# Performance work log

Hardware: AMD Instinct MI355X
Metric: run time of the kernel (lower is better)

Reference implementation:

```python
import jax, jax.numpy as jnp
import numpy as np

N_NODES = 100000
N_EDGES = 3200000
IN_CH = 32
HID = 16


def setup_inputs() -> dict:
    key = jax.random.key(0)
    ks = jax.random.split(key, 8)
    x = jax.random.normal(ks[0], (N_NODES, IN_CH), dtype=jnp.float32)
    edge_index = jax.random.randint(ks[1], (2, N_EDGES), 0, N_NODES, dtype=jnp.int64)
    s1 = 1.0 / np.sqrt(IN_CH)
    s2 = 1.0 / np.sqrt(HID)
    Wl1 = jax.random.normal(ks[2], (HID, IN_CH), dtype=jnp.float32) * s1
    Wr1 = jax.random.normal(ks[3], (HID, IN_CH), dtype=jnp.float32) * s1
    b1 = jnp.zeros((HID,), dtype=jnp.float32)
    Wl2 = jax.random.normal(ks[4], (1, HID), dtype=jnp.float32) * s2
    Wr2 = jax.random.normal(ks[5], (1, HID), dtype=jnp.float32) * s2
    b2 = jnp.zeros((1,), dtype=jnp.float32)
    return {"x": x, "edge_index": edge_index, "Wl1": Wl1, "Wr1": Wr1,
            "b1": b1, "Wl2": Wl2, "Wr2": Wr2, "b2": b2}


def _sage_conv(h, src, dst, deg_inv, Wl, Wr, b):
    # mean aggregation of source features at destination nodes
    msg_sum = jax.ops.segment_sum(h[src], dst, num_segments=N_NODES)  # [N, F]
    agg = msg_sum * deg_inv[:, None]
    # lin_l(agg) + lin_r(h): lin_l carries the bias (PyG SAGEConv convention)
    return agg @ Wl.T + b + h @ Wr.T


def reference(x, edge_index, Wl1, Wr1, b1, Wl2, Wr2, b2):
    src = edge_index[0]
    dst = edge_index[1]
    deg = jax.ops.segment_sum(jnp.ones((N_EDGES,), dtype=x.dtype), dst,
                              num_segments=N_NODES)
    deg_inv = 1.0 / jnp.maximum(deg, 1.0)  # mean; nodes w/o in-edges get 0 agg

    h = _sage_conv(x, src, dst, deg_inv, Wl1, Wr1, b1)
    h = jax.nn.relu(h)
    # F.dropout in eval mode -> identity
    out = _sage_conv(h, src, dst, deg_inv, Wl2, Wr2, b2)
    return out.squeeze(-1)  # [N]
```

## Files before the change

### kernel.cpp

```cpp
#include <hip/hip_runtime.h>

#define N_NODES 100000
#define N_EDGES 3200000
#define NB 768
#define BKN 131
#define RSZ 5120
#define TILE 6250
#define NTILES 512
#define MAXIT 13
#define MAXB 10


__device__ __forceinline__ float bf2f_lo(unsigned int w) {
  return __uint_as_float(w << 16);
}
__device__ __forceinline__ float bf2f_hi(unsigned int w) {
  return __uint_as_float(w & 0xFFFF0000u);
}
__device__ __forceinline__ unsigned short f2bf(float f) {
  unsigned int b = __float_as_uint(f);
  return (unsigned short)((b + 0x7FFFu + ((b >> 16) & 1u)) >> 16);
}

__global__ __launch_bounds__(256) void k_proj1(
    const float* __restrict__ x, const float* __restrict__ Wl1,
    const float* __restrict__ Wr1, const float* __restrict__ b1,
    unsigned short* __restrict__ p1h, float* __restrict__ q1b,
    int* __restrict__ gcur) {
  __shared__ float sWl[512];
  __shared__ float sWr[512];
  __shared__ float sb[16];
  const int t = threadIdx.x;
  if (t < 32) {
    const int gi = blockIdx.x * 32 + t;
    if (gi < NB * 16) gcur[gi] = 0;
  }
  for (int i = t; i < 512; i += 256) {
    sWl[i] = Wl1[i];
    sWr[i] = Wr1[i];
  }
  if (t < 16) sb[t] = b1[t];
  __syncthreads();

  const int n = blockIdx.x * 256 + t;
  if (n >= N_NODES) return;

  float xr[32];
  const float4* xp = (const float4*)(x + (size_t)n * 32);
#pragma unroll
  for (int j = 0; j < 8; ++j) {
    float4 v = xp[j];
    xr[4 * j + 0] = v.x;
    xr[4 * j + 1] = v.y;
    xr[4 * j + 2] = v.z;
    xr[4 * j + 3] = v.w;
  }
  float pv[16], qv[16];
#pragma unroll
  for (int hh = 0; hh < 16; ++hh) {
    float a = 0.f, b = 0.f;
#pragma unroll
    for (int i = 0; i < 32; ++i) {
      a = fmaf(xr[i], sWl[hh * 32 + i], a);
      b = fmaf(xr[i], sWr[hh * 32 + i], b);
    }
    pv[hh] = a;
    qv[hh] = b + sb[hh];
  }
  unsigned int w[8];
#pragma unroll
  for (int j = 0; j < 8; ++j)
    w[j] = (unsigned int)f2bf(pv[2 * j]) |
           ((unsigned int)f2bf(pv[2 * j + 1]) << 16);
  uint4* pp = (uint4*)(p1h + (size_t)n * 16);
  pp[0] = make_uint4(w[0], w[1], w[2], w[3]);
  pp[1] = make_uint4(w[4], w[5], w[6], w[7]);
  float4* qp = (float4*)(q1b + (size_t)n * 16);
#pragma unroll
  for (int j = 0; j < 4; ++j)
    qp[j] = make_float4(qv[4 * j], qv[4 * j + 1], qv[4 * j + 2], qv[4 * j + 3]);
}

__global__ __launch_bounds__(512) void k_bscatter(const int* __restrict__ ei,
                                                  int* __restrict__ gcur,
                                                  int* __restrict__ recs) {
  __shared__ int hist[1024];
  __shared__ int delta[NB];
  __shared__ int seg[512];
  __shared__ int stage[TILE];
  __shared__ unsigned short bid[TILE + 6];
  const int t = threadIdx.x;
  for (int i = t; i < 1024; i += 512) hist[i] = 0;
  __syncthreads();

  const int tb = blockIdx.x * TILE;
  int rec[MAXIT], aux[MAXIT];
#pragma unroll
  for (int i = 0; i < MAXIT; ++i) {
    const int pos = t + i * 512;
    if (pos < TILE) {
      const int e = tb + pos;
      const int s = ei[e];
      const int d = ei[N_EDGES + e];
      const int k = (int)((unsigned)d / (unsigned)BKN);
      const int rank = atomicAdd(&hist[k], 1);
      rec[i] = ((d - k * BKN) << 17) | s;
      aux[i] = (k << 16) | rank;
    } else {
      aux[i] = -1;
    }
  }
  __syncthreads();

  const int s0 = hist[2 * t], s1 = hist[2 * t + 1];
  const int my = s0 + s1;
  seg[t] = my;
  __syncthreads();
#pragma unroll
  for (int o = 1; o < 512; o <<= 1) {
    const int a = (t >= o) ? seg[t - o] : 0;
    __syncthreads();
    seg[t] += a;
    __syncthreads();
  }
  const int ex = seg[t] - my;
  hist[2 * t] = ex;
  hist[2 * t + 1] = ex + s0;
  {
    const int b = 2 * t;
    if (b < NB && s0) delta[b] = b * RSZ + atomicAdd(&gcur[b * 16], s0) - ex;
    if (b + 1 < NB && s1)
      delta[b + 1] =
          (b + 1) * RSZ + atomicAdd(&gcur[(b + 1) * 16], s1) - (ex + s0);
  }
  __syncthreads();

#pragma unroll
  for (int i = 0; i < MAXIT; ++i) {
    if (aux[i] >= 0) stage[hist[aux[i] >> 16] + (aux[i] & 0xFFFF)] = rec[i];
  }
  for (int k2 = t; k2 < NB; k2 += 512) {
    const int st = hist[k2];
    const int en = hist[k2 + 1];
    for (int p = st; p < en; ++p) bid[p] = (unsigned short)k2;
  }
  __syncthreads();

  for (int pos = t; pos < TILE; pos += 512) {
    const int idx = delta[bid[pos]] + pos;
    if ((unsigned)idx < (unsigned)(NB * RSZ)) recs[idx] = stage[pos];
  }
}

__global__ __launch_bounds__(512) void k_sortagg1(
    const int* __restrict__ gcur, int* __restrict__ recs,
    const unsigned short* __restrict__ p1h, const float* __restrict__ q1b,
    const float* __restrict__ Wl2, const float* __restrict__ Wr2,
    float* __restrict__ p2, float* __restrict__ r2,
    float* __restrict__ deg_inv, int* __restrict__ node_off,
    int* __restrict__ node_cnt) {
  __shared__ int hist[132];
  __shared__ int nstart[132];
  __shared__ int ssort[RSZ];
  __shared__ float sWl[16], sWr[16];
  const int t = threadIdx.x;
  const int kb = blockIdx.x;
  const int b0 = kb * RSZ;
  const int gend = b0 + min(gcur[kb * 16], RSZ);
  if (t < 132) hist[t] = 0;
  if (t < 16) {
    sWl[t] = Wl2[t];
    sWr[t] = Wr2[t];
  }
  __syncthreads();

  int rc[MAXB], ax[MAXB];
#pragma unroll
  for (int i = 0; i < MAXB; ++i) {
    const int r = b0 + t + i * 512;
    if (r < gend) {
      const int rec = recs[r];
      const int local = rec >> 17;
      const int rank = atomicAdd(&hist[local], 1);
      rc[i] = rec & 0x1FFFF;
      ax[i] = (local << 13) | rank;
    } else {
      ax[i] = -1;
    }
  }
  __syncthreads();

  {
    int v = (t < 132) ? hist[t] : 0;
    if (t < 132) nstart[t] = v;
    __syncthreads();
#pragma unroll
    for (int o = 1; o < 132; o <<= 1) {
      const int a = (t < 132 && t >= o) ? nstart[t - o] : 0;
      __syncthreads();
      if (t < 132) nstart[t] += a;
      __syncthreads();
    }
    if (t < 132) nstart[t] -= v;
  }
  __syncthreads();

#pragma unroll
  for (int i = 0; i < MAXB; ++i) {
    if (ax[i] >= 0) ssort[nstart[ax[i] >> 13] + (ax[i] & 0x1FFF)] = rc[i];
  }
  __syncthreads();

  const int T = gend - b0;
  for (int j2 = t; j2 < T; j2 += 512) recs[b0 + j2] = ssort[j2];
  if (t < BKN) {
    const int n2 = kb * BKN + t;
    node_off[n2] = b0 + nstart[t];
    node_cnt[n2] = hist[t];
  }

  const int quad = t & 3;
  const int half = quad & 1;
  const int epar = quad >> 1;
  const unsigned short* pb = p1h + half * 8;
#pragma unroll
  for (int p = 0; p < 2; ++p) {
    const int local = p * 128 + (t >> 2);
    if (local >= BKN) continue;
    const int n = kb * BKN + local;
    if (n >= N_NODES) continue;
    const int st = nstart[local];
    const int k = hist[local];

    float acc[8];
#pragma unroll
    for (int i = 0; i < 8; ++i) acc[i] = 0.f;
    int j = epar;
    for (; j + 6 < k; j += 8) {
      const int s0 = ssort[st + j], s1 = ssort[st + j + 2],
                s2 = ssort[st + j + 4], s3 = ssort[st + j + 6];
      const uint4 w0 = *(const uint4*)(pb + (size_t)s0 * 16);
      const uint4 w1 = *(const uint4*)(pb + (size_t)s1 * 16);
      const uint4 w2 = *(const uint4*)(pb + (size_t)s2 * 16);
      const uint4 w3 = *(const uint4*)(pb + (size_t)s3 * 16);
      acc[0] +=
          (bf2f_lo(w0.x) + bf2f_lo(w1.x)) + (bf2f_lo(w2.x) + bf2f_lo(w3.x));
      acc[1] +=
          (bf2f_hi(w0.x) + bf2f_hi(w1.x)) + (bf2f_hi(w2.x) + bf2f_hi(w3.x));
      acc[2] +=
          (bf2f_lo(w0.y) + bf2f_lo(w1.y)) + (bf2f_lo(w2.y) + bf2f_lo(w3.y));
      acc[3] +=
          (bf2f_hi(w0.y) + bf2f_hi(w1.y)) + (bf2f_hi(w2.y) + bf2f_hi(w3.y));
      acc[4] +=
          (bf2f_lo(w0.z) + bf2f_lo(w1.z)) + (bf2f_lo(w2.z) + bf2f_lo(w3.z));
      acc[5] +=
          (bf2f_hi(w0.z) + bf2f_hi(w1.z)) + (bf2f_hi(w2.z) + bf2f_hi(w3.z));
      acc[6] +=
          (bf2f_lo(w0.w) + bf2f_lo(w1.w)) + (bf2f_lo(w2.w) + bf2f_lo(w3.w));
      acc[7] +=
          (bf2f_hi(w0.w) + bf2f_hi(w1.w)) + (bf2f_hi(w2.w) + bf2f_hi(w3.w));
    }
    for (; j < k; j += 2) {
      const uint4 w = *(const uint4*)(pb + (size_t)ssort[st + j] * 16);
      acc[0] += bf2f_lo(w.x);
      acc[1] += bf2f_hi(w.x);
      acc[2] += bf2f_lo(w.y);
      acc[3] += bf2f_hi(w.y);
      acc[4] += bf2f_lo(w.z);
      acc[5] += bf2f_hi(w.z);
      acc[6] += bf2f_lo(w.w);
      acc[7] += bf2f_hi(w.w);
    }
#pragma unroll
    for (int i = 0; i < 8; ++i) acc[i] += __shfl_xor(acc[i], 2);

    const float di = 1.f / fmaxf((float)k, 1.f);
    const float4* qp = (const float4*)(q1b + (size_t)n * 16 + half * 8);
    const float4 qa = qp[0], qb = qp[1];
    float h[8];
    h[0] = fmaxf(fmaf(acc[0], di, qa.x), 0.f);
    h[1] = fmaxf(fmaf(acc[1], di, qa.y), 0.f);
    h[2] = fmaxf(fmaf(acc[2], di, qa.z), 0.f);
    h[3] = fmaxf(fmaf(acc[3], di, qa.w), 0.f);
    h[4] = fmaxf(fmaf(acc[4], di, qb.x), 0.f);
    h[5] = fmaxf(fmaf(acc[5], di, qb.y), 0.f);
    h[6] = fmaxf(fmaf(acc[6], di, qb.z), 0.f);
    h[7] = fmaxf(fmaf(acc[7], di, qb.w), 0.f);
    float pa = 0.f, pbv = 0.f;
#pragma unroll
    for (int i = 0; i < 8; ++i) {
      pa = fmaf(h[i], sWl[half * 8 + i], pa);
      pbv = fmaf(h[i], sWr[half * 8 + i], pbv);
    }
    pa += __shfl_xor(pa, 1);
    pbv += __shfl_xor(pbv, 1);
    if (quad == 0) {
      p2[n] = pa;
      r2[n] = pbv;
      deg_inv[n] = di;
    }
  }
}

__global__ __launch_bounds__(512) void k_agg2out(
    const int* __restrict__ node_off, const int* __restrict__ node_cnt,
    const int* __restrict__ recs, const float* __restrict__ p2,
    const float* __restrict__ r2, const float* __restrict__ deg_inv,
    const float* __restrict__ b2, float* __restrict__ out) {
  const int t = threadIdx.x;
  const int kb = blockIdx.x;
  const int quad = t & 3;
#pragma unroll
  for (int p = 0; p < 2; ++p) {
    const int local = p * 128 + (t >> 2);
    if (local >= BKN) continue;
    const int n = kb * BKN + local;
    if (n >= N_NODES) continue;
    const int k0 = node_off[n];
    const int k = node_cnt[n];
    const int* sl = recs + k0;

    float u = 0.f;
    int j = quad;
    for (; j + 12 < k; j += 16) {
      const int sA = sl[j], sB = sl[j + 4], sC = sl[j + 8], sD = sl[j + 12];
      u += (p2[sA] + p2[sB]) + (p2[sC] + p2[sD]);
    }
    for (; j < k; j += 4) u += p2[sl[j]];
    u += __shfl_xor(u, 1);
    u += __shfl_xor(u, 2);
    if (quad == 0) out[n] = fmaf(u, deg_inv[n], r2[n] + b2[0]);
  }
}

extern "C" void kernel_launch(void* const* d_in, const int* in_sizes, int n_in,
                              void* d_out, int out_size, void* d_ws,
                              size_t ws_size, hipStream_t stream) {
  const float* x   = (const float*)d_in[0];
  const int*   ei  = (const int*)d_in[1];
  const float* Wl1 = (const float*)d_in[2];
  const float* Wr1 = (const float*)d_in[3];
  const float* b1  = (const float*)d_in[4];
  const float* Wl2 = (const float*)d_in[5];
  const float* Wr2 = (const float*)d_in[6];
  const float* b2  = (const float*)d_in[7];
  float* out = (float*)d_out;

  const size_t N = N_NODES;
  int* wi = (int*)d_ws;
  int* gcur     = wi;
  int* node_off = wi + NB * 16;
  int* node_cnt = node_off + 100608;
  int* recs     = node_cnt + 100608;
  unsigned short* p1h = (unsigned short*)(recs + (size_t)NB * RSZ);
  float* q1b     = (float*)(p1h + 16 * N);
  float* p2      = q1b + 16 * N;
  float* r2      = p2 + N;
  float* deg_inv = r2 + N;

  k_proj1<<<(N_NODES + 255) / 256, 256, 0, stream>>>(x, Wl1, Wr1, b1, p1h,
                                                     q1b, gcur);
  k_bscatter<<<NTILES, 512, 0, stream>>>(ei, gcur, recs);
  k_sortagg1<<<NB, 512, 0, stream>>>(gcur, recs, p1h, q1b, Wl2, Wr2, p2, r2,
                                     deg_inv, node_off, node_cnt);
  k_agg2out<<<NB, 512, 0, stream>>>(node_off, node_cnt, recs, p2, r2, deg_inv,
                                    b2, out);
}
```

Measured before the change: 175.0 us.

## Fuse pipeline into one cooperative kernel with grid syncs and shared-memory handoff

Merges the projection, bucket scatter, per-bucket sort/aggregation and second-layer aggregation into a single cooperative kernel of 512 blocks that are separated by grid-wide syncs. Buckets are resized to 196 nodes so one block handles one bucket and one edge tile. The sorted source lists, degrees and r2 values stay in shared memory for the final phase, so the sorted records and node offsets are never written back to global memory. This is meant to remove three kernel launch gaps and that global round trip. In exchange it depends on cooperative launch succeeding with large shared-memory usage, and falls back to three separate kernels if it does not.

Result: slower. 501.2 us (+186.3%).

```diff
diff --git a/kernel.cpp b/kernel.cpp
--- a/kernel.cpp
+++ b/kernel.cpp
@@ -1,15 +1,36 @@
 #include <hip/hip_runtime.h>
+#include <hip/hip_cooperative_groups.h>
+
+namespace cg = cooperative_groups;
 
 #define N_NODES 100000
 #define N_EDGES 3200000
-#define NB 768
-#define BKN 131
-#define RSZ 5120
+#define NB2 512
+#define BKN2 196
+#define RSZ2 7424
 #define TILE 6250
-#define NTILES 512
 #define MAXIT 13
-#define MAXB 10
-
+#define MAXB2 15
+
+
+union SM {
+  struct { float sWl[512]; float sWr[512]; float sb[16]; } proj;
+  struct {
+    int hist[1024];
+    int delta[NB2];
+    int seg[512];
+    int stage[TILE];
+    unsigned short bid[TILE + 6];
+  } sc;
+  struct {
+    int hist[BKN2 + 4];
+    int nstart[BKN2 + 4];
+    float sWl2[16], sWr2[16];
+    float sdeg[BKN2];
+    float sr2[BKN2];
+    int ssort[RSZ2];
+  } so;
+};
 
 __device__ __forceinline__ float bf2f_lo(unsigned int w) {
   return __uint_as_float(w << 16);
@@ -22,78 +43,65 @@
   return (unsigned short)((b + 0x7FFFu + ((b >> 16) & 1u)) >> 16);
 }
 
-__global__ __launch_bounds__(256) void k_proj1(
-    const float* __restrict__ x, const float* __restrict__ Wl1,
-    const float* __restrict__ Wr1, const float* __restrict__ b1,
-    unsigned short* __restrict__ p1h, float* __restrict__ q1b,
-    int* __restrict__ gcur) {
-  __shared__ float sWl[512];
-  __shared__ float sWr[512];
-  __shared__ float sb[16];
+__device__ __forceinline__ void phaseA(
+    const float* __restrict__ x, const int* __restrict__ ei,
+    const float* __restrict__ Wl1, const float* __restrict__ Wr1,
+    const float* __restrict__ b1, unsigned short* __restrict__ p1h,
+    float* __restrict__ q1b, int* __restrict__ gcur, int* __restrict__ recs,
+    SM& sm) {
   const int t = threadIdx.x;
-  if (t < 32) {
-    const int gi = blockIdx.x * 32 + t;
-    if (gi < NB * 16) gcur[gi] = 0;
-  }
-  for (int i = t; i < 512; i += 256) {
-    sWl[i] = Wl1[i];
-    sWr[i] = Wr1[i];
-  }
-  if (t < 16) sb[t] = b1[t];
-  __syncthreads();
-
-  const int n = blockIdx.x * 256 + t;
-  if (n >= N_NODES) return;
-
-  float xr[32];
-  const float4* xp = (const float4*)(x + (size_t)n * 32);
-#pragma unroll
-  for (int j = 0; j < 8; ++j) {
-    float4 v = xp[j];
-    xr[4 * j + 0] = v.x;
-    xr[4 * j + 1] = v.y;
-    xr[4 * j + 2] = v.z;
-    xr[4 * j + 3] = v.w;
-  }
-  float pv[16], qv[16];
-#pragma unroll
-  for (int hh = 0; hh < 16; ++hh) {
-    float a = 0.f, b = 0.f;
-#pragma unroll
-    for (int i = 0; i < 32; ++i) {
-      a = fmaf(xr[i], sWl[hh * 32 + i], a);
-      b = fmaf(xr[i], sWr[hh * 32 + i], b);
-    }
-    pv[hh] = a;
-    qv[hh] = b + sb[hh];
-  }
-  unsigned int w[8];
-#pragma unroll
-  for (int j = 0; j < 8; ++j)
-    w[j] = (unsigned int)f2bf(pv[2 * j]) |
-           ((unsigned int)f2bf(pv[2 * j + 1]) << 16);
-  uint4* pp = (uint4*)(p1h + (size_t)n * 16);
-  pp[0] = make_uint4(w[0], w[1], w[2], w[3]);
-  pp[1] = make_uint4(w[4], w[5], w[6], w[7]);
-  float4* qp = (float4*)(q1b + (size_t)n * 16);
-#pragma unroll
-  for (int j = 0; j < 4; ++j)
-    qp[j] = make_float4(qv[4 * j], qv[4 * j + 1], qv[4 * j + 2], qv[4 * j + 3]);
-}
-
-__global__ __launch_bounds__(512) void k_bscatter(const int* __restrict__ ei,
-                                                  int* __restrict__ gcur,
-                                                  int* __restrict__ recs) {
-  __shared__ int hist[1024];
-  __shared__ int delta[NB];
-  __shared__ int seg[512];
-  __shared__ int stage[TILE];
-  __shared__ unsigned short bid[TILE + 6];
-  const int t = threadIdx.x;
-  for (int i = t; i < 1024; i += 512) hist[i] = 0;
-  __syncthreads();
-
-  const int tb = blockIdx.x * TILE;
+  const int kb = blockIdx.x;
+
+  sm.proj.sWl[t] = Wl1[t];
+  sm.proj.sWr[t] = Wr1[t];
+  if (t < 16) sm.proj.sb[t] = b1[t];
+  __syncthreads();
+  if (t < BKN2) {
+    const int n = kb * BKN2 + t;
+    if (n < N_NODES) {
+      float xr[32];
+      const float4* xp = (const float4*)(x + (size_t)n * 32);
+#pragma unroll
+      for (int j = 0; j < 8; ++j) {
+        float4 v = xp[j];
+        xr[4 * j + 0] = v.x;
+        xr[4 * j + 1] = v.y;
+        xr[4 * j + 2] = v.z;
+        xr[4 * j + 3] = v.w;
+      }
+      float pv[16], qv[16];
+#pragma unroll
+      for (int hh = 0; hh < 16; ++hh) {
+        float a = 0.f, b = 0.f;
+#pragma unroll
+        for (int i = 0; i < 32; ++i) {
+          a = fmaf(xr[i], sm.proj.sWl[hh * 32 + i], a);
+          b = fmaf(xr[i], sm.proj.sWr[hh * 32 + i], b);
+        }
+        pv[hh] = a;
+        qv[hh] = b + sm.proj.sb[hh];
+      }
+      unsigned int w[8];
+#pragma unroll
+      for (int j = 0; j < 8; ++j)
+        w[j] = (unsigned int)f2bf(pv[2 * j]) |
+               ((unsigned int)f2bf(pv[2 * j + 1]) << 16);
+      uint4* pp = (uint4*)(p1h + (size_t)n * 16);
+      pp[0] = make_uint4(w[0], w[1], w[2], w[3]);
+      pp[1] = make_uint4(w[4], w[5], w[6], w[7]);
+      float4* qp = (float4*)(q1b + (size_t)n * 16);
+#pragma unroll
+      for (int j = 0; j < 4; ++j)
+        qp[j] =
+            make_float4(qv[4 * j], qv[4 * j + 1], qv[4 * j + 2], qv[4 * j + 3]);
+    }
+  }
+  __syncthreads();
+
+  for (int i = t; i < 1024; i += 512) sm.sc.hist[i] = 0;
+  __syncthreads();
+
+  const int tb = kb * TILE;
   int rec[MAXIT], aux[MAXIT];
 #pragma unroll
   for (int i = 0; i < MAXIT; ++i) {
@@ -102,9 +110,9 @@
       const int e = tb + pos;
       const int s = ei[e];
       const int d = ei[N_EDGES + e];
-      const int k = (int)((unsigned)d / (unsigned)BKN);
-      const int rank = atomicAdd(&hist[k], 1);
-      rec[i] = ((d - k * BKN) << 17) | s;
+      const int k = (int)((unsigned)d / (unsigned)BKN2);
+      const int rank = atomicAdd(&sm.sc.hist[k], 1);
+      rec[i] = ((d - k * BKN2) << 17) | s;
       aux[i] = (k << 16) | rank;
     } else {
       aux[i] = -1;
@@ -112,77 +120,77 @@
   }
   __syncthreads();
 
-  const int s0 = hist[2 * t], s1 = hist[2 * t + 1];
+  const int s0 = sm.sc.hist[2 * t], s1 = sm.sc.hist[2 * t + 1];
   const int my = s0 + s1;
-  seg[t] = my;
+  sm.sc.seg[t] = my;
   __syncthreads();
 #pragma unroll
   for (int o = 1; o < 512; o <<= 1) {
-    const int a = (t >= o) ? seg[t - o] : 0;
+    const int a = (t >= o) ? sm.sc.seg[t - o] : 0;
     __syncthreads();
-    seg[t] += a;
+    sm.sc.seg[t] += a;
     __syncthreads();
   }
-  const int ex = seg[t] - my;
-  hist[2 * t] = ex;
-  hist[2 * t + 1] = ex + s0;
+  const int ex = sm.sc.seg[t] - my;
+  sm.sc.hist[2 * t] = ex;
+  sm.sc.hist[2 * t + 1] = ex + s0;
   {
     const int b = 2 * t;
-    if (b < NB && s0) delta[b] = b * RSZ + atomicAdd(&gcur[b * 16], s0) - ex;
-    if (b + 1 < NB && s1)
-      delta[b + 1] =
-          (b + 1) * RSZ + atomicAdd(&gcur[(b + 1) * 16], s1) - (ex + s0);
+    if (b < NB2 && s0)
+      sm.sc.delta[b] = b * RSZ2 + atomicAdd(&gcur[b * 16], s0) - ex;
+    if (b + 1 < NB2 && s1)
+      sm.sc.delta[b + 1] =
+          (b + 1) * RSZ2 + atomicAdd(&gcur[(b + 1) * 16], s1) - (ex + s0);
   }
   __syncthreads();
 
 #pragma unroll
   for (int i = 0; i < MAXIT; ++i) {
-    if (aux[i] >= 0) stage[hist[aux[i] >> 16] + (aux[i] & 0xFFFF)] = rec[i];
-  }
-  for (int k2 = t; k2 < NB; k2 += 512) {
-    const int st = hist[k2];
-    const int en = hist[k2 + 1];
-    for (int p = st; p < en; ++p) bid[p] = (unsigned short)k2;
+    if (aux[i] >= 0)
+      sm.sc.stage[sm.sc.hist[aux[i] >> 16] + (aux[i] & 0xFFFF)] = rec[i];
+  }
+  {
+    const int st = sm.sc.hist[t];
+    const int en = sm.sc.hist[t + 1];
+    for (int p = st; p < en; ++p) sm.sc.bid[p] = (unsigned short)t;
   }
   __syncthreads();
 
   for (int pos = t; pos < TILE; pos += 512) {
-    const int idx = delta[bid[pos]] + pos;
-    if ((unsigned)idx < (unsigned)(NB * RSZ)) recs[idx] = stage[pos];
-  }
-}
-
-__global__ __launch_bounds__(512) void k_sortagg1(
+    const int bb = sm.sc.bid[pos];
+    const int idx = sm.sc.delta[bb] + pos;
+    if (idx < (bb + 1) * RSZ2) recs[idx] = sm.sc.stage[pos];
+  }
+}
+
+template <bool FUSED>
+__device__ __forceinline__ void phaseB(
     const int* __restrict__ gcur, int* __restrict__ recs,
     const unsigned short* __restrict__ p1h, const float* __restrict__ q1b,
     const float* __restrict__ Wl2, const float* __restrict__ Wr2,
-    float* __restrict__ p2, float* __restrict__ r2,
-    float* __restrict__ deg_inv, int* __restrict__ node_off,
-    int* __restrict__ node_cnt) {
-  __shared__ int hist[132];
-  __shared__ int nstart[132];
-  __shared__ int ssort[RSZ];
-  __shared__ float sWl[16], sWr[16];
+    float* __restrict__ p2, float* __restrict__ r2g, float* __restrict__ degg,
+    int* __restrict__ node_off, int* __restrict__ node_cnt, SM& sm) {
   const int t = threadIdx.x;
   const int kb = blockIdx.x;
-  const int b0 = kb * RSZ;
-  const int gend = b0 + min(gcur[kb * 16], RSZ);
-  if (t < 132) hist[t] = 0;
+  const int b0 = kb * RSZ2;
+  const int cnt = min(gcur[kb * 16], RSZ2);
+  const int gend = b0 + cnt;
+  if (t < BKN2 + 4) sm.so.hist[t] = 0;
   if (t < 16) {
-    sWl[t] = Wl2[t];
-    sWr[t] = Wr2[t];
-  }
-  __syncthreads();
-
-  int rc[MAXB], ax[MAXB];
-#pragma unroll
-  for (int i = 0; i < MAXB; ++i) {
+    sm.so.sWl2[t] = Wl2[t];
+    sm.so.sWr2[t] = Wr2[t];
+  }
+  __syncthreads();
+
+  int rc[MAXB2], ax[MAXB2];
+#pragma unroll
+  for (int i = 0; i < MAXB2; ++i) {
     const int r = b0 + t + i * 512;
     if (r < gend) {
-      const int rec = recs[r];
-      const int local = rec >> 17;
-      const int rank = atomicAdd(&hist[local], 1);
-      rc[i] = rec & 0x1FFFF;
+      const int rv = recs[r];
+      const int local = rv >> 17;
+      const int rank = atomicAdd(&sm.so.hist[local], 1);
+      rc[i] = rv & 0x1FFFF;
       ax[i] = (local << 13) | rank;
     } else {
       ax[i] = -1;
@@ -191,32 +199,36 @@
   __syncthreads();
 
   {
-    int v = (t < 132) ? hist[t] : 0;
-    if (t < 132) nstart[t] = v;
+    int v = (t <= BKN2) ? sm.so.hist[t] : 0;
+    if (t <= BKN2) sm.so.nstart[t] = v;
     __syncthreads();
 #pragma unroll
-    for (int o = 1; o < 132; o <<= 1) {
-      const int a = (t < 132 && t >= o) ? nstart[t - o] : 0;
+    for (int o = 1; o < BKN2 + 1; o <<= 1) {
+      const int a = (t <= BKN2 && t >= o) ? sm.so.nstart[t - o] : 0;
       __syncthreads();
-      if (t < 132) nstart[t] += a;
+      if (t <= BKN2) sm.so.nstart[t] += a;
       __syncthreads();
     }
-    if (t < 132) nstart[t] -= v;
-  }
-  __syncthreads();
-
-#pragma unroll
-  for (int i = 0; i < MAXB; ++i) {
-    if (ax[i] >= 0) ssort[nstart[ax[i] >> 13] + (ax[i] & 0x1FFF)] = rc[i];
-  }
-  __syncthreads();
-
-  const int T = gend - b0;
-  for (int j2 = t; j2 < T; j2 += 512) recs[b0 + j2] = ssort[j2];
-  if (t < BKN) {
-    const int n2 = kb * BKN + t;
-    node_off[n2] = b0 + nstart[t];
-    node_cnt[n2] = hist[t];
+    if (t <= BKN2) sm.so.nstart[t] -= v;
+  }
+  __syncthreads();
+
+#pragma unroll
+  for (int i = 0; i < MAXB2; ++i) {
+    if (ax[i] >= 0)
+      sm.so.ssort[sm.so.nstart[ax[i] >> 13] + (ax[i] & 0x1FFF)] = rc[i];
+  }
+  __syncthreads();
+
+  if (!FUSED) {
+    for (int j2 = t; j2 < cnt; j2 += 512) recs[b0 + j2] = sm.so.ssort[j2];
+    if (t < BKN2) {
+      const int n2 = kb * BKN2 + t;
+      if (n2 < N_NODES) {
+        node_off[n2] = b0 + sm.so.nstart[t];
+        node_cnt[n2] = sm.so.hist[t];
+      }
+    }
   }
 
   const int quad = t & 3;
@@ -226,19 +238,19 @@
 #pragma unroll
   for (int p = 0; p < 2; ++p) {
     const int local = p * 128 + (t >> 2);
-    if (local >= BKN) continue;
-    const int n = kb * BKN + local;
+    if (local >= BKN2) continue;
+    const int n = kb * BKN2 + local;
     if (n >= N_NODES) continue;
-    const int st = nstart[local];
-    const int k = hist[local];
+    const int st = sm.so.nstart[local];
+    const int k = sm.so.hist[local];
 
     float acc[8];
 #pragma unroll
     for (int i = 0; i < 8; ++i) acc[i] = 0.f;
     int j = epar;
     for (; j + 6 < k; j += 8) {
-      const int s0 = ssort[st + j], s1 = ssort[st + j + 2],
-                s2 = ssort[st + j + 4], s3 = ssort[st + j + 6];
+      const int s0 = sm.so.ssort[st + j], s1 = sm.so.ssort[st + j + 2],
+                s2 = sm.so.ssort[st + j + 4], s3 = sm.so.ssort[st + j + 6];
       const uint4 w0 = *(const uint4*)(pb + (size_t)s0 * 16);
       const uint4 w1 = *(const uint4*)(pb + (size_t)s1 * 16);
       const uint4 w2 = *(const uint4*)(pb + (size_t)s2 * 16);
@@ -261,7 +273,7 @@
           (bf2f_hi(w0.w) + bf2f_hi(w1.w)) + (bf2f_hi(w2.w) + bf2f_hi(w3.w));
     }
     for (; j < k; j += 2) {
-      const uint4 w = *(const uint4*)(pb + (size_t)ssort[st + j] * 16);
+      const uint4 w = *(const uint4*)(pb + (size_t)sm.so.ssort[st + j] * 16);
       acc[0] += bf2f_lo(w.x);
       acc[1] += bf2f_hi(w.x);
       acc[2] += bf2f_lo(w.y);
@@ -289,80 +301,156 @@
     float pa = 0.f, pbv = 0.f;
 #pragma unroll
     for (int i = 0; i < 8; ++i) {
-      pa = fmaf(h[i], sWl[half * 8 + i], pa);
-      pbv = fmaf(h[i], sWr[half * 8 + i], pbv);
+      pa = fmaf(h[i], sm.so.sWl2[half * 8 + i], pa);
+      pbv = fmaf(h[i], sm.so.sWr2[half * 8 + i], pbv);
     }
     pa += __shfl_xor(pa, 1);
     pbv += __shfl_xor(pbv, 1);
     if (quad == 0) {
       p2[n] = pa;
-      r2[n] = pbv;
-      deg_inv[n] = di;
-    }
-  }
-}
-
-__global__ __launch_bounds__(512) void k_agg2out(
+      if (FUSED) {
+        sm.so.sr2[local] = pbv;
+        sm.so.sdeg[local] = di;
+      } else {
+        r2g[n] = pbv;
+        degg[n] = di;
+      }
+    }
+  }
+}
+
+template <bool FUSED>
+__device__ __forceinline__ void phaseC(
     const int* __restrict__ node_off, const int* __restrict__ node_cnt,
     const int* __restrict__ recs, const float* __restrict__ p2,
-    const float* __restrict__ r2, const float* __restrict__ deg_inv,
-    const float* __restrict__ b2, float* __restrict__ out) {
+    const float* __restrict__ r2g, const float* __restrict__ degg,
+    const float* __restrict__ b2, float* __restrict__ out, SM& sm) {
   const int t = threadIdx.x;
   const int kb = blockIdx.x;
   const int quad = t & 3;
+  const float bias = b2[0];
 #pragma unroll
   for (int p = 0; p < 2; ++p) {
     const int local = p * 128 + (t >> 2);
-    if (local >= BKN) continue;
-    const int n = kb * BKN + local;
+    if (local >= BKN2) continue;
+    const int n = kb * BKN2 + local;
     if (n >= N_NODES) continue;
-    const int k0 = node_off[n];
-    const int k = node_cnt[n];
-    const int* sl = recs + k0;
+    int st, k;
+    if (FUSED) {
+      st = sm.so.nstart[local];
+      k = sm.so.hist[local];
+    } else {
+      st = node_off[n];
+      k = node_cnt[n];
+    }
 
     float u = 0.f;
     int j = quad;
-    for (; j + 12 < k; j += 16) {
-      const int sA = sl[j], sB = sl[j + 4], sC = sl[j + 8], sD = sl[j + 12];
-      u += (p2[sA] + p2[sB]) + (p2[sC] + p2[sD]);
-    }
-    for (; j < k; j += 4) u += p2[sl[j]];
+    if (FUSED) {
+      for (; j + 12 < k; j += 16) {
+        const int sA = sm.so.ssort[st + j], sB = sm.so.ssort[st + j + 4],
+                  sC = sm.so.ssort[st + j + 8], sD = sm.so.ssort[st + j + 12];
+        u += (p2[sA] + p2[sB]) + (p2[sC] + p2[sD]);
+      }
+      for (; j < k; j += 4) u += p2[sm.so.ssort[st + j]];
+    } else {
+      const int* sl = recs + st;
+      for (; j + 12 < k; j += 16) {
+        const int sA = sl[j], sB = sl[j + 4], sC = sl[j + 8], sD = sl[j + 12];
+        u += (p2[sA] + p2[sB]) + (p2[sC] + p2[sD]);
+      }
+      for (; j < k; j += 4) u += p2[sl[j]];
+    }
     u += __shfl_xor(u, 1);
     u += __shfl_xor(u, 2);
-    if (quad == 0) out[n] = fmaf(u, deg_inv[n], r2[n] + b2[0]);
-  }
+    if (quad == 0) {
+      const float di = FUSED ? sm.so.sdeg[local] : degg[n];
+      const float rv = FUSED ? sm.so.sr2[local] : r2g[n];
+      out[n] = fmaf(u, di, rv + bias);
+    }
+  }
+}
+
+__global__ __launch_bounds__(512, 4) void k_fused(
+    const float* x, const int* ei, const float* Wl1, const float* Wr1,
+    const float* b1, const float* Wl2, const float* Wr2, const float* b2,
+    unsigned short* p1h, float* q1b, int* gcur, int* recs, float* p2,
+    float* out) {
+  __shared__ SM sm;
+  cg::grid_group g = cg::this_grid();
+  phaseA(x, ei, Wl1, Wr1, b1, p1h, q1b, gcur, recs, sm);
+  __threadfence();
+  g.sync();
+  phaseB<true>(gcur, recs, p1h, q1b, Wl2, Wr2, p2, nullptr, nullptr, nullptr,
+               nullptr, sm);
+  __threadfence();
+  g.sync();
+  phaseC<true>(nullptr, nullptr, recs, p2, nullptr, nullptr, b2, out, sm);
+}
+
+__global__ __launch_bounds__(512, 4) void k_pA(const float* x, const int* ei,
+                                               const float* Wl1,
+                                               const float* Wr1,
+                                               const float* b1,
+                                               unsigned short* p1h, float* q1b,
+                                               int* gcur, int* recs) {
+  __shared__ SM sm;
+  phaseA(x, ei, Wl1, Wr1, b1, p1h, q1b, gcur, recs, sm);
+}
+__global__ __launch_bounds__(512, 4) void k_pB(
+    const int* gcur, int* recs, const unsigned short* p1h, const float* q1b,
+    const float* Wl2, const float* Wr2, float* p2, float* r2g, float* degg,
+    int* node_off, int* node_cnt) {
+  __shared__ SM sm;
+  phaseB<false>(gcur, recs, p1h, q1b, Wl2, Wr2, p2, r2g, degg, node_off,
+                node_cnt, sm);
+}
+__global__ __launch_bounds__(512, 4) void k_pC(
+    const int* node_off, const int* node_cnt, const int* recs, const float* p2,
+    const float* r2g, const float* degg, const float* b2, float* out) {
+  __shared__ SM sm;
+  phaseC<false>(node_off, node_cnt, recs, p2, r2g, degg, b2, out, sm);
 }
 
 extern "C" void kernel_launch(void* const* d_in, const int* in_sizes, int n_in,
                               void* d_out, int out_size, void* d_ws,
                               size_t ws_size, hipStream_t stream) {
-  const float* x   = (const float*)d_in[0];
-  const int*   ei  = (const int*)d_in[1];
+  const float* x = (const float*)d_in[0];
+  const int* ei = (const int*)d_in[1];
   const float* Wl1 = (const float*)d_in[2];
   const float* Wr1 = (const float*)d_in[3];
-  const float* b1  = (const float*)d_in[4];
+  const float* b1 = (const float*)d_in[4];
   const float* Wl2 = (const float*)d_in[5];
   const float* Wr2 = (const float*)d_in[6];
-  const float* b2  = (const float*)d_in[7];
+  const float* b2 = (const float*)d_in[7];
   float* out = (float*)d_out;
 
   const size_t N = N_NODES;
   int* wi = (int*)d_ws;
-  int* gcur     = wi;
-  int* node_off = wi + NB * 16;
-  int* node_cnt = node_off + 100608;
-  int* recs     = node_cnt + 100608;
-  unsigned short* p1h = (unsigned short*)(recs + (size_t)NB * RSZ);
-  float* q1b     = (float*)(p1h + 16 * N);
-  float* p2      = q1b + 16 * N;
-  float* r2      = p2 + N;
-  float* deg_inv = r2 + N;
-
-  k_proj1<<<(N_NODES + 255) / 256, 256, 0, stream>>>(x, Wl1, Wr1, b1, p1h,
-                                                     q1b, gcur);
-  k_bscatter<<<NTILES, 512, 0, stream>>>(ei, gcur, recs);
-  k_sortagg1<<<NB, 512, 0, stream>>>(gcur, recs, p1h, q1b, Wl2, Wr2, p2, r2,
-                                     deg_inv, node_off, node_cnt);
-  k_agg2out<<<NB, 512, 0, stream>>>(node_off, node_cnt, recs, p2, r2, deg_inv,
-                                    b2, out);
-}
+  int* gcur = wi;
+  int* node_off = wi + NB2 * 16;
+  int* node_cnt = node_off + 100352;
+  int* recs = node_cnt + 100352;
+  unsigned short* p1h = (unsigned short*)(recs + (size_t)NB2 * RSZ2);
+  float* q1b = (float*)(p1h + 16 * N);
+  float* p2 = q1b + 16 * N;
+  float* r2 = p2 + N;
+  float* degg = r2 + N;
+
+  hipMemsetAsync(gcur, 0, NB2 * 16 * sizeof(int), stream);
+
+  void* ka[] = {(void*)&x,   (void*)&ei,  (void*)&Wl1, (void*)&Wr1,
+                (void*)&b1,  (void*)&Wl2, (void*)&Wr2, (void*)&b2,
+                (void*)&p1h, (void*)&q1b, (void*)&gcur, (void*)&recs,
+                (void*)&p2,  (void*)&out};
+  hipError_t err = hipLaunchCooperativeKernel(
+      reinterpret_cast<void*>(k_fused), dim3(NB2), dim3(512), ka, 0, stream);
+  if (err != hipSuccess) {
+    (void)hipGetLastError();
+    k_pA<<<NB2, 512, 0, stream>>>(x, ei, Wl1, Wr1, b1, p1h, q1b, gcur, recs);
+    k_pB<<<NB2, 512, 0, stream>>>(gcur, recs, p1h, q1b, Wl2, Wr2, p2, r2, degg,
+                                  node_off, node_cnt);
+    k_pC<<<NB2, 512, 0, stream>>>(node_off, node_cnt, recs, p2, r2, degg, b2,
+                                  out);
+  }
+}
```

## Use smaller buckets and LDS-atomic layer-2 aggregation over unsorted records

Applied to the files above, without the earlier changes.

Grows the bucket count to 1024 with 98 nodes per bucket and a smaller record region per bucket. Each sort/aggregate block now handles one node per quad, and the block no longer writes sorted records and per-node offsets back to global memory. Layer-2 aggregation reads the unsorted bucket records directly and accumulates p2 values with shared-memory atomics per local node. This drops a global write-back pass and two index arrays, at the cost of shared atomic contention and a tighter per-bucket capacity that could overflow on skewed inputs.

Result: no change. 172.0 us (-1.7%).

```diff
diff --git a/kernel.cpp b/kernel.cpp
--- a/kernel.cpp
+++ b/kernel.cpp
@@ -2,13 +2,13 @@
 
 #define N_NODES 100000
 #define N_EDGES 3200000
-#define NB 768
-#define BKN 131
-#define RSZ 5120
+#define NB 1024
+#define BKN 98
+#define RSZ 3968
 #define TILE 6250
 #define NTILES 512
 #define MAXIT 13
-#define MAXB 10
+#define MAXB 8
 
 
 __device__ __forceinline__ float bf2f_lo(unsigned int w) {
@@ -31,8 +31,8 @@
   __shared__ float sWr[512];
   __shared__ float sb[16];
   const int t = threadIdx.x;
-  if (t < 32) {
-    const int gi = blockIdx.x * 32 + t;
+  if (t < 64) {
+    const int gi = blockIdx.x * 64 + t;
     if (gi < NB * 16) gcur[gi] = 0;
   }
   for (int i = t; i < 512; i += 256) {
@@ -128,8 +128,8 @@
   hist[2 * t + 1] = ex + s0;
   {
     const int b = 2 * t;
-    if (b < NB && s0) delta[b] = b * RSZ + atomicAdd(&gcur[b * 16], s0) - ex;
-    if (b + 1 < NB && s1)
+    if (s0) delta[b] = b * RSZ + atomicAdd(&gcur[b * 16], s0) - ex;
+    if (s1)
       delta[b + 1] =
           (b + 1) * RSZ + atomicAdd(&gcur[(b + 1) * 16], s1) - (ex + s0);
   }
@@ -141,33 +141,33 @@
   }
   for (int k2 = t; k2 < NB; k2 += 512) {
     const int st = hist[k2];
-    const int en = hist[k2 + 1];
+    const int en = (k2 == NB - 1) ? TILE : hist[k2 + 1];
     for (int p = st; p < en; ++p) bid[p] = (unsigned short)k2;
   }
   __syncthreads();
 
   for (int pos = t; pos < TILE; pos += 512) {
-    const int idx = delta[bid[pos]] + pos;
-    if ((unsigned)idx < (unsigned)(NB * RSZ)) recs[idx] = stage[pos];
-  }
-}
-
-__global__ __launch_bounds__(512) void k_sortagg1(
-    const int* __restrict__ gcur, int* __restrict__ recs,
+    const int bb = bid[pos];
+    const int idx = delta[bb] + pos;
+    if (idx < (bb + 1) * RSZ) recs[idx] = stage[pos];
+  }
+}
+
+__global__ __launch_bounds__(512, 8) void k_sortagg1(
+    const int* __restrict__ gcur, const int* __restrict__ recs,
     const unsigned short* __restrict__ p1h, const float* __restrict__ q1b,
     const float* __restrict__ Wl2, const float* __restrict__ Wr2,
     float* __restrict__ p2, float* __restrict__ r2,
-    float* __restrict__ deg_inv, int* __restrict__ node_off,
-    int* __restrict__ node_cnt) {
-  __shared__ int hist[132];
-  __shared__ int nstart[132];
+    float* __restrict__ deg_inv) {
+  __shared__ int hist[128];
+  __shared__ int nstart[128];
   __shared__ int ssort[RSZ];
   __shared__ float sWl[16], sWr[16];
   const int t = threadIdx.x;
   const int kb = blockIdx.x;
   const int b0 = kb * RSZ;
   const int gend = b0 + min(gcur[kb * 16], RSZ);
-  if (t < 132) hist[t] = 0;
+  if (t < 128) hist[t] = 0;
   if (t < 16) {
     sWl[t] = Wl2[t];
     sWr[t] = Wr2[t];
@@ -179,10 +179,10 @@
   for (int i = 0; i < MAXB; ++i) {
     const int r = b0 + t + i * 512;
     if (r < gend) {
-      const int rec = recs[r];
-      const int local = rec >> 17;
+      const int rv = recs[r];
+      const int local = rv >> 17;
       const int rank = atomicAdd(&hist[local], 1);
-      rc[i] = rec & 0x1FFFF;
+      rc[i] = rv & 0x1FFFF;
       ax[i] = (local << 13) | rank;
     } else {
       ax[i] = -1;
@@ -191,17 +191,17 @@
   __syncthreads();
 
   {
-    int v = (t < 132) ? hist[t] : 0;
-    if (t < 132) nstart[t] = v;
+    const int v = (t < 128) ? hist[t] : 0;
+    if (t < 128) nstart[t] = v;
     __syncthreads();
 #pragma unroll
-    for (int o = 1; o < 132; o <<= 1) {
-      const int a = (t < 132 && t >= o) ? nstart[t - o] : 0;
+    for (int o = 1; o < 128; o <<= 1) {
+      const int a = (t < 128 && t >= o) ? nstart[t - o] : 0;
       __syncthreads();
-      if (t < 132) nstart[t] += a;
+      if (t < 128) nstart[t] += a;
       __syncthreads();
     }
-    if (t < 132) nstart[t] -= v;
+    if (t < 128) nstart[t] -= v;
   }
   __syncthreads();
 
@@ -210,126 +210,126 @@
     if (ax[i] >= 0) ssort[nstart[ax[i] >> 13] + (ax[i] & 0x1FFF)] = rc[i];
   }
   __syncthreads();
-
-  const int T = gend - b0;
-  for (int j2 = t; j2 < T; j2 += 512) recs[b0 + j2] = ssort[j2];
-  if (t < BKN) {
-    const int n2 = kb * BKN + t;
-    node_off[n2] = b0 + nstart[t];
-    node_cnt[n2] = hist[t];
-  }
 
   const int quad = t & 3;
   const int half = quad & 1;
   const int epar = quad >> 1;
   const unsigned short* pb = p1h + half * 8;
-#pragma unroll
-  for (int p = 0; p < 2; ++p) {
-    const int local = p * 128 + (t >> 2);
-    if (local >= BKN) continue;
+  const int local = t >> 2;
+  if (local < BKN) {
     const int n = kb * BKN + local;
-    if (n >= N_NODES) continue;
-    const int st = nstart[local];
-    const int k = hist[local];
-
-    float acc[8];
-#pragma unroll
-    for (int i = 0; i < 8; ++i) acc[i] = 0.f;
-    int j = epar;
-    for (; j + 6 < k; j += 8) {
-      const int s0 = ssort[st + j], s1 = ssort[st + j + 2],
-                s2 = ssort[st + j + 4], s3 = ssort[st + j + 6];
-      const uint4 w0 = *(const uint4*)(pb + (size_t)s0 * 16);
-      const uint4 w1 = *(const uint4*)(pb + (size_t)s1 * 16);
-      const uint4 w2 = *(const uint4*)(pb + (size_t)s2 * 16);
-      const uint4 w3 = *(const uint4*)(pb + (size_t)s3 * 16);
-      acc[0] +=
-          (bf2f_lo(w0.x) + bf2f_lo(w1.x)) + (bf2f_lo(w2.x) + bf2f_lo(w3.x));
-      acc[1] +=
-          (bf2f_hi(w0.x) + bf2f_hi(w1.x)) + (bf2f_hi(w2.x) + bf2f_hi(w3.x));
-      acc[2] +=
-          (bf2f_lo(w0.y) + bf2f_lo(w1.y)) + (bf2f_lo(w2.y) + bf2f_lo(w3.y));
-      acc[3] +=
-          (bf2f_hi(w0.y) + bf2f_hi(w1.y)) + (bf2f_hi(w2.y) + bf2f_hi(w3.y));
-      acc[4] +=
-          (bf2f_lo(w0.z) + bf2f_lo(w1.z)) + (bf2f_lo(w2.z) + bf2f_lo(w3.z));
-      acc[5] +=
-          (bf2f_hi(w0.z) + bf2f_hi(w1.z)) + (bf2f_hi(w2.z) + bf2f_hi(w3.z));
-      acc[6] +=
-          (bf2f_lo(w0.w) + bf2f_lo(w1.w)) + (bf2f_lo(w2.w) + bf2f_lo(w3.w));
-      acc[7] +=
-          (bf2f_hi(w0.w) + bf2f_hi(w1.w)) + (bf2f_hi(w2.w) + bf2f_hi(w3.w));
-    }
-    for (; j < k; j += 2) {
-      const uint4 w = *(const uint4*)(pb + (size_t)ssort[st + j] * 16);
-      acc[0] += bf2f_lo(w.x);
-      acc[1] += bf2f_hi(w.x);
-      acc[2] += bf2f_lo(w.y);
-      acc[3] += bf2f_hi(w.y);
-      acc[4] += bf2f_lo(w.z);
-      acc[5] += bf2f_hi(w.z);
-      acc[6] += bf2f_lo(w.w);
-      acc[7] += bf2f_hi(w.w);
-    }
-#pragma unroll
-    for (int i = 0; i < 8; ++i) acc[i] += __shfl_xor(acc[i], 2);
-
-    const float di = 1.f / fmaxf((float)k, 1.f);
-    const float4* qp = (const float4*)(q1b + (size_t)n * 16 + half * 8);
-    const float4 qa = qp[0], qb = qp[1];
-    float h[8];
-    h[0] = fmaxf(fmaf(acc[0], di, qa.x), 0.f);
-    h[1] = fmaxf(fmaf(acc[1], di, qa.y), 0.f);
-    h[2] = fmaxf(fmaf(acc[2], di, qa.z), 0.f);
-    h[3] = fmaxf(fmaf(acc[3], di, qa.w), 0.f);
-    h[4] = fmaxf(fmaf(acc[4], di, qb.x), 0.f);
-    h[5] = fmaxf(fmaf(acc[5], di, qb.y), 0.f);
-    h[6] = fmaxf(fmaf(acc[6], di, qb.z), 0.f);
-    h[7] = fmaxf(fmaf(acc[7], di, qb.w), 0.f);
-    float pa = 0.f, pbv = 0.f;
-#pragma unroll
-    for (int i = 0; i < 8; ++i) {
-      pa = fmaf(h[i], sWl[half * 8 + i], pa);
-      pbv = fmaf(h[i], sWr[half * 8 + i], pbv);
-    }
-    pa += __shfl_xor(pa, 1);
-    pbv += __shfl_xor(pbv, 1);
-    if (quad == 0) {
-      p2[n] = pa;
-      r2[n] = pbv;
-      deg_inv[n] = di;
-    }
-  }
-}
-
-__global__ __launch_bounds__(512) void k_agg2out(
-    const int* __restrict__ node_off, const int* __restrict__ node_cnt,
-    const int* __restrict__ recs, const float* __restrict__ p2,
-    const float* __restrict__ r2, const float* __restrict__ deg_inv,
-    const float* __restrict__ b2, float* __restrict__ out) {
+    if (n < N_NODES) {
+      const int st = nstart[local];
+      const int k = hist[local];
+
+      float acc[8];
+#pragma unroll
+      for (int i = 0; i < 8; ++i) acc[i] = 0.f;
+      int j = epar;
+      for (; j + 6 < k; j += 8) {
+        const int s0 = ssort[st + j], s1 = ssort[st + j + 2],
+                  s2 = ssort[st + j + 4], s3 = ssort[st + j + 6];
+        const uint4 w0 = *(const uint4*)(pb + (size_t)s0 * 16);
+        const uint4 w1 = *(const uint4*)(pb + (size_t)s1 * 16);
+        const uint4 w2 = *(const uint4*)(pb + (size_t)s2 * 16);
+        const uint4 w3 = *(const uint4*)(pb + (size_t)s3 * 16);
+        acc[0] +=
+            (bf2f_lo(w0.x) + bf2f_lo(w1.x)) + (bf2f_lo(w2.x) + bf2f_lo(w3.x));
+        acc[1] +=
+            (bf2f_hi(w0.x) + bf2f_hi(w1.x)) + (bf2f_hi(w2.x) + bf2f_hi(w3.x));
+        acc[2] +=
+            (bf2f_lo(w0.y) + bf2f_lo(w1.y)) + (bf2f_lo(w2.y) + bf2f_lo(w3.y));
+        acc[3] +=
+            (bf2f_hi(w0.y) + bf2f_hi(w1.y)) + (bf2f_hi(w2.y) + bf2f_hi(w3.y));
+        acc[4] +=
+            (bf2f_lo(w0.z) + bf2f_lo(w1.z)) + (bf2f_lo(w2.z) + bf2f_lo(w3.z));
+        acc[5] +=
+            (bf2f_hi(w0.z) + bf2f_hi(w1.z)) + (bf2f_hi(w2.z) + bf2f_hi(w3.z));
+        acc[6] +=
+            (bf2f_lo(w0.w) + bf2f_lo(w1.w)) + (bf2f_lo(w2.w) + bf2f_lo(w3.w));
+        acc[7] +=
+            (bf2f_hi(w0.w) + bf2f_hi(w1.w)) + (bf2f_hi(w2.w) + bf2f_hi(w3.w));
+      }
+      for (; j < k; j += 2) {
+        const uint4 w = *(const uint4*)(pb + (size_t)ssort[st + j] * 16);
+        acc[0] += bf2f_lo(w.x);
+        acc[1] += bf2f_hi(w.x);
+        acc[2] += bf2f_lo(w.y);
+        acc[3] += bf2f_hi(w.y);
+        acc[4] += bf2f_lo(w.z);
+        acc[5] += bf2f_hi(w.z);
+        acc[6] += bf2f_lo(w.w);
+        acc[7] += bf2f_hi(w.w);
+      }
+#pragma unroll
+      for (int i = 0; i < 8; ++i) acc[i] += __shfl_xor(acc[i], 2);
+
+      const float di = 1.f / fmaxf((float)k, 1.f);
+      const float4* qp = (const float4*)(q1b + (size_t)n * 16 + half * 8);
+      const float4 qa = qp[0], qb = qp[1];
+      float h[8];
+      h[0] = fmaxf(fmaf(acc[0], di, qa.x), 0.f);
+      h[1] = fmaxf(fmaf(acc[1], di, qa.y), 0.f);
+      h[2] = fmaxf(fmaf(acc[2], di, qa.z), 0.f);
+      h[3] = fmaxf(fmaf(acc[3], di, qa.w), 0.f);
+      h[4] = fmaxf(fmaf(acc[4], di, qb.x), 0.f);
+      h[5] = fmaxf(fmaf(acc[5], di, qb.y), 0.f);
+      h[6] = fmaxf(fmaf(acc[6], di, qb.z), 0.f);
+      h[7] = fmaxf(fmaf(acc[7], di, qb.w), 0.f);
+      float pa = 0.f, pbv = 0.f;
+#pragma unroll
+      for (int i = 0; i < 8; ++i) {
+        pa = fmaf(h[i], sWl[half * 8 + i], pa);
+        pbv = fmaf(h[i], sWr[half * 8 + i], pbv);
+      }
+      pa += __shfl_xor(pa, 1);
+      pbv += __shfl_xor(pbv, 1);
+      if (quad == 0) {
+        p2[n] = pa;
+        r2[n] = pbv;
+        deg_inv[n] = di;
+      }
+    }
+  }
+}
+
+__global__ __launch_bounds__(512, 8) void k_agg2out(
+    const int* __restrict__ gcur, const int* __restrict__ recs,
+    const float* __restrict__ p2, const float* __restrict__ r2,
+    const float* __restrict__ deg_inv, const float* __restrict__ b2,
+    float* __restrict__ out) {
+  __shared__ float acc[BKN];
   const int t = threadIdx.x;
   const int kb = blockIdx.x;
-  const int quad = t & 3;
-#pragma unroll
-  for (int p = 0; p < 2; ++p) {
-    const int local = p * 128 + (t >> 2);
-    if (local >= BKN) continue;
-    const int n = kb * BKN + local;
-    if (n >= N_NODES) continue;
-    const int k0 = node_off[n];
-    const int k = node_cnt[n];
-    const int* sl = recs + k0;
-
-    float u = 0.f;
-    int j = quad;
-    for (; j + 12 < k; j += 16) {
-      const int sA = sl[j], sB = sl[j + 4], sC = sl[j + 8], sD = sl[j + 12];
-      u += (p2[sA] + p2[sB]) + (p2[sC] + p2[sD]);
-    }
-    for (; j < k; j += 4) u += p2[sl[j]];
-    u += __shfl_xor(u, 1);
-    u += __shfl_xor(u, 2);
-    if (quad == 0) out[n] = fmaf(u, deg_inv[n], r2[n] + b2[0]);
+  if (t < BKN) acc[t] = 0.f;
+  __syncthreads();
+
+  const int b0 = kb * RSZ;
+  const int cnt = min(gcur[kb * 16], RSZ);
+  int r = t;
+  for (; r + 1536 < cnt; r += 2048) {
+    const int rv0 = recs[b0 + r];
+    const int rv1 = recs[b0 + r + 512];
+    const int rv2 = recs[b0 + r + 1024];
+    const int rv3 = recs[b0 + r + 1536];
+    const float v0 = p2[rv0 & 0x1FFFF];
+    const float v1 = p2[rv1 & 0x1FFFF];
+    const float v2 = p2[rv2 & 0x1FFFF];
+    const float v3 = p2[rv3 & 0x1FFFF];
+    atomicAdd(&acc[rv0 >> 17], v0);
+    atomicAdd(&acc[rv1 >> 17], v1);
+    atomicAdd(&acc[rv2 >> 17], v2);
+    atomicAdd(&acc[rv3 >> 17], v3);
+  }
+  for (; r < cnt; r += 512) {
+    const int rv = recs[b0 + r];
+    atomicAdd(&acc[rv >> 17], p2[rv & 0x1FFFF]);
+  }
+  __syncthreads();
+
+  if (t < BKN) {
+    const int n = kb * BKN + t;
+    if (n < N_NODES) out[n] = fmaf(acc[t], deg_inv[n], r2[n] + b2[0]);
   }
 }
 
@@ -348,10 +348,8 @@
 
   const size_t N = N_NODES;
   int* wi = (int*)d_ws;
-  int* gcur     = wi;
-  int* node_off = wi + NB * 16;
-  int* node_cnt = node_off + 100608;
-  int* recs     = node_cnt + 100608;
+  int* gcur = wi;
+  int* recs = wi + NB * 16;
   unsigned short* p1h = (unsigned short*)(recs + (size_t)NB * RSZ);
   float* q1b     = (float*)(p1h + 16 * N);
   float* p2      = q1b + 16 * N;
@@ -362,7 +360,6 @@
                                                      q1b, gcur);
   k_bscatter<<<NTILES, 512, 0, stream>>>(ei, gcur, recs);
   k_sortagg1<<<NB, 512, 0, stream>>>(gcur, recs, p1h, q1b, Wl2, Wr2, p2, r2,
-                                     deg_inv, node_off, node_cnt);
-  k_agg2out<<<NB, 512, 0, stream>>>(node_off, node_cnt, recs, p2, r2, deg_inv,
-                                    b2, out);
-}
+                                     deg_inv);
+  k_agg2out<<<NB, 512, 0, stream>>>(gcur, recs, p2, r2, deg_inv, b2, out);
+}
```
